# Kernel optimization log

Hardware: AMD Instinct MI355X
Metric: run time of the kernel (lower is better)

## Reference

```python
import jax, jax.numpy as jnp
import numpy as np

D_MODEL = 1024
D_STATE = 16  # hardcoded in original: A = randn(d_model, 16)


def setup_inputs() -> dict:
    key = jax.random.key(0)
    ks = jax.random.split(key, 9)
    D = D_MODEL
    s = 1.0 / np.sqrt(D)
    x = jax.random.normal(ks[0], (4, 8192, D), dtype=jnp.float32)
    in_w = jax.random.uniform(ks[1], (2 * D, D), minval=-s, maxval=s, dtype=jnp.float32)
    in_b = jax.random.uniform(ks[2], (2 * D,), minval=-s, maxval=s, dtype=jnp.float32)
    out_w = jax.random.uniform(ks[3], (D, D), minval=-s, maxval=s, dtype=jnp.float32)
    out_b = jax.random.uniform(ks[4], (D,), minval=-s, maxval=s, dtype=jnp.float32)
    dt_w = jax.random.uniform(ks[5], (D, D), minval=-s, maxval=s, dtype=jnp.float32)
    dt_b = jax.random.uniform(ks[6], (D,), minval=-s, maxval=s, dtype=jnp.float32)
    A = jax.random.normal(ks[7], (D, D_STATE), dtype=jnp.float32)
    Dp = jax.random.normal(ks[8], (D,), dtype=jnp.float32)
    return {"x": x, "in_w": in_w, "in_b": in_b, "out_w": out_w, "out_b": out_b,
            "dt_w": dt_w, "dt_b": dt_b, "A": A, "Dp": Dp}


def reference(x, in_w, in_b, out_w, out_b, dt_w, dt_b, A, Dp):
    # x: [B, L, D]. in_proj -> [B, L, 2D], split into x_val / res.
    x_and_res = jnp.einsum('bld,ed->ble', x, in_w) + in_b
    x_val, res = jnp.split(x_and_res, 2, axis=-1)
    # Original computes dt = softplus(dt_proj(xt)) per timestep but never uses it
    # (dead compute, A/Dp/h also unused); output depends only on silu gating.
    # y_t = xt * sigmoid(xt) == silu(x_val), fully parallel over L (no recurrence).
    y = x_val * jax.nn.sigmoid(x_val)
    gated = y * jax.nn.silu(res)
    return jnp.einsum('bld,ed->ble', gated, out_w) + out_b
```

## Files before the change

kernel.cpp:

```cpp
#include <hip/hip_runtime.h>
#include <cstdint>


typedef __bf16 bf16x8 __attribute__((ext_vector_type(8)));
typedef float f32x4 __attribute__((ext_vector_type(4)));

#define KD 1024
#define NT 32
#define BUF_ELEMS 16384

__device__ __forceinline__ void gload_lds16(const void* g, void* lds_u) {
  __builtin_amdgcn_global_load_lds(
      (__attribute__((address_space(1))) void*)(uintptr_t)g,
      (__attribute__((address_space(3))) void*)(uint32_t)(uintptr_t)lds_u,
      16, 0, 0);
}

__device__ __forceinline__ float silu_f(float v) {
  return v / (1.0f + __expf(-v));
}

#define WAITB(N) do { \
  asm volatile("s_waitcnt vmcnt(" #N ")" ::: "memory"); \
  asm volatile("s_barrier" ::: "memory"); } while (0)

__global__ void cast_f32_to_bf16_x8(const float* __restrict__ in,
                                    __bf16* __restrict__ out, int n8) {
  int i = blockIdx.x * blockDim.x + threadIdx.x;
  if (i >= n8) return;
  const float4* p = (const float4*)in;
  float4 v0 = p[2 * i];
  float4 v1 = p[2 * i + 1];
  bf16x8 o;
  o[0] = (__bf16)v0.x; o[1] = (__bf16)v0.y; o[2] = (__bf16)v0.z; o[3] = (__bf16)v0.w;
  o[4] = (__bf16)v1.x; o[5] = (__bf16)v1.y; o[6] = (__bf16)v1.z; o[7] = (__bf16)v1.w;
  ((bf16x8*)out)[i] = o;
}

__global__ void cast_w1_interleave(const float* __restrict__ in,
                                   __bf16* __restrict__ out) {
  int i = blockIdx.x * blockDim.x + threadIdx.x;
  int orow = i >> 7;
  int chunk = i & 127;
  int srow = (orow >> 1) + ((orow & 1) << 10);
  const float4* p = (const float4*)(in + ((size_t)srow << 10) + (chunk << 3));
  float4 v0 = p[0], v1 = p[1];
  bf16x8 o;
  o[0] = (__bf16)v0.x; o[1] = (__bf16)v0.y; o[2] = (__bf16)v0.z; o[3] = (__bf16)v0.w;
  o[4] = (__bf16)v1.x; o[5] = (__bf16)v1.y; o[6] = (__bf16)v1.z; o[7] = (__bf16)v1.w;
  *(bf16x8*)(out + ((size_t)orow << 10) + (chunk << 3)) = o;
}

template <int BUF>
__device__ __forceinline__ void stage_tile(const __bf16*& pa, const __bf16*& pb,
                                           __bf16* smw) {
  __bf16* d = smw + BUF * BUF_ELEMS;
  gload_lds16(pa, d);
  gload_lds16(pa + 128 * KD, d + 4096);
  gload_lds16(pb, d + 8192);
  gload_lds16(pb + 128 * KD, d + 12288);
  pa += 32;
  pb += 32;
}

template <int BUF>
__device__ __forceinline__ void compute_tile(const __bf16* sm, int aoff, int boff,
                                             f32x4 (&acc)[8][4]) {
  const __bf16* base = sm + BUF * BUF_ELEMS;
  bf16x8 af[8], bf[4];
#pragma unroll
  for (int i = 0; i < 8; ++i)
    af[i] = *(const bf16x8*)(base + aoff + i * 512);
#pragma unroll
  for (int j = 0; j < 4; ++j)
    bf[j] = *(const bf16x8*)(base + boff + j * 512);
  __builtin_amdgcn_s_setprio(1);
#pragma unroll
  for (int i = 0; i < 8; ++i)
#pragma unroll
    for (int j = 0; j < 4; ++j)
      acc[i][j] = __builtin_amdgcn_mfma_f32_16x16x32_bf16(af[i], bf[j], acc[i][j], 0, 0, 0);
  __builtin_amdgcn_s_setprio(0);
}

__device__ __forceinline__ void gemm_core(const __bf16* __restrict__ A,
                                          const __bf16* __restrict__ B,
                                          __bf16* sm, long m0, long n0,
                                          f32x4 (&acc)[8][4]) {
  const int t = threadIdx.x;
  const int w = t >> 6;
  const int lane = t & 63;
  const int lr = lane & 15;
  const int lk = lane >> 4;
  const int wr = w >> 2;
  const int wc = w & 3;

  const int l = lane;
  const int stg_row = w * 16 + (l >> 2);
  const int stg_col = ((l & 3) ^ ((l >> 3) & 3)) << 3;
  const __bf16* pa = A + (m0 + stg_row) * KD + stg_col;
  const __bf16* pb = B + (n0 + stg_row) * KD + stg_col;
  __bf16* smw = sm + w * 512;

  const int swz8 = (lk ^ ((lr >> 1) & 3)) << 3;
  const int aoff = (wr * 128 + lr) * 32 + swz8;
  const int boff = 8192 + (wc * 64 + lr) * 32 + swz8;

#pragma unroll
  for (int i = 0; i < 8; ++i)
#pragma unroll
    for (int j = 0; j < 4; ++j)
      acc[i][j] = (f32x4){0.f, 0.f, 0.f, 0.f};

  stage_tile<0>(pa, pb, smw);
  stage_tile<1>(pa, pb, smw);

  for (int it = 0; it < 10; ++it) {
    WAITB(4); stage_tile<2>(pa, pb, smw); compute_tile<0>(sm, aoff, boff, acc);
    WAITB(4); stage_tile<0>(pa, pb, smw); compute_tile<1>(sm, aoff, boff, acc);
    WAITB(4); stage_tile<1>(pa, pb, smw); compute_tile<2>(sm, aoff, boff, acc);
  }
  WAITB(4); compute_tile<0>(sm, aoff, boff, acc);
  WAITB(0); compute_tile<1>(sm, aoff, boff, acc);
}

__global__ __launch_bounds__(512, 2)
void gemm1_silu(const __bf16* __restrict__ X, const __bf16* __restrict__ W1i,
                const float* __restrict__ in_b, __bf16* __restrict__ G) {
  __shared__ __bf16 sm[3 * BUF_ELEMS];
  const int bid = blockIdx.x;
  const int swz = (bid & 7) * 128 + (bid >> 3);
  const int m_idx = swz >> 3;
  const int n_idx = swz & 7;
  const long m0 = (long)m_idx * 256;
  const long n0 = (long)n_idx * 256;

  f32x4 acc[8][4];
  gemm_core(X, W1i, sm, m0, n0, acc);

  const int lane = threadIdx.x & 63;
  const int w = threadIdx.x >> 6;
  const int wr = w >> 2, wc = w & 3;

  float bj[4];
#pragma unroll
  for (int j = 0; j < 4; ++j) {
    int nn = (int)n0 + wc * 64 + j * 16 + (lane & 15);
    bj[j] = (nn & 1) ? in_b[1024 + (nn >> 1)] : in_b[nn >> 1];
  }
#pragma unroll
  for (int i = 0; i < 8; ++i)
#pragma unroll
    for (int j = 0; j < 4; ++j)
#pragma unroll
      for (int q = 0; q < 4; ++q) {
        int r = wr * 128 + i * 16 + (lane >> 4) * 4 + q;
        float v = acc[i][j][q] + bj[j];
        float s = silu_f(v);
        float p = __shfl_xor(s, 1);
        float g = s * p;
        if (!(lane & 1)) {
          int nn = (int)n0 + wc * 64 + j * 16 + (lane & 15);
          G[(m0 + r) * 1024 + (nn >> 1)] = (__bf16)g;
        }
      }
}

__global__ __launch_bounds__(512, 2)
void gemm2_bias(const __bf16* __restrict__ G, const __bf16* __restrict__ W2,
                const float* __restrict__ out_b, float* __restrict__ OUT) {
  __shared__ __bf16 sm[3 * BUF_ELEMS];
  const int bid = blockIdx.x;
  const int swz = (bid & 7) * 64 + (bid >> 3);
  const int m_idx = swz >> 2;
  const int n_idx = swz & 3;
  const long m0 = (long)m_idx * 256;
  const long n0 = (long)n_idx * 256;

  f32x4 acc[8][4];
  gemm_core(G, W2, sm, m0, n0, acc);

  const int lane = threadIdx.x & 63;
  const int w = threadIdx.x >> 6;
  const int wr = w >> 2, wc = w & 3;

  float ob[4];
#pragma unroll
  for (int j = 0; j < 4; ++j)
    ob[j] = out_b[(int)n0 + wc * 64 + j * 16 + (lane & 15)];
#pragma unroll
  for (int i = 0; i < 8; ++i)
#pragma unroll
    for (int j = 0; j < 4; ++j)
#pragma unroll
      for (int q = 0; q < 4; ++q) {
        int r = wr * 128 + i * 16 + (lane >> 4) * 4 + q;
        int c = wc * 64 + j * 16 + (lane & 15);
        OUT[(m0 + r) * 1024 + n0 + c] = acc[i][j][q] + ob[j];
      }
}

extern "C" void kernel_launch(void* const* d_in, const int* in_sizes, int n_in,
                              void* d_out, int out_size, void* d_ws, size_t ws_size,
                              hipStream_t stream) {
  const float* x = (const float*)d_in[0];
  const float* in_w = (const float*)d_in[1];
  const float* in_b = (const float*)d_in[2];
  const float* out_w = (const float*)d_in[3];
  const float* out_b = (const float*)d_in[4];

  char* ws = (char*)d_ws;
  __bf16* xb = (__bf16*)(ws);
  __bf16* w1b = (__bf16*)(ws + (size_t)67108864);
  __bf16* w2b = (__bf16*)(ws + (size_t)71303168);
  __bf16* gb = (__bf16*)(ws + (size_t)73400320);

  cast_f32_to_bf16_x8<<<dim3(16384), 256, 0, stream>>>(x, xb, 33554432 / 8);
  cast_w1_interleave<<<dim3(1024), 256, 0, stream>>>(in_w, w1b);
  cast_f32_to_bf16_x8<<<dim3(512), 256, 0, stream>>>(out_w, w2b, 1048576 / 8);

  gemm1_silu<<<dim3(1024), 512, 0, stream>>>(xb, w1b, in_b, gb);
  gemm2_bias<<<dim3(512), 512, 0, stream>>>(gb, w2b, out_b, (float*)d_out);
}
```

Baseline: 291.7 us.

## Restructure GEMM mainloop to BK=64 double-buffer with phased MFMA/LDS interleave

Replaces the triple-buffered BK=32 pipeline with a double-buffered BK=64 scheme. Each K-tile is split into four barrier-delimited phases that interleave LDS fragment reads, global-to-LDS staging of the next tile, and MFMA bursts at raised priority. A new XOR swizzle fits the 64-wide rows. The aim is fewer barriers per K step and better overlap of loads with MFMA. In exchange it uses 128KB of LDS per block, which may drop the two-blocks-per-CU occupancy the launch bounds ask for, and it adds more barriers inside each tile.

After: 288.0 us. No clear change (-1.3%).

```diff
diff --git a/kernel.cpp b/kernel.cpp
--- a/kernel.cpp
+++ b/kernel.cpp
@@ -6,8 +6,6 @@
 typedef float f32x4 __attribute__((ext_vector_type(4)));
 
 #define KD 1024
-#define NT 32
-#define BUF_ELEMS 16384
 
 __device__ __forceinline__ void gload_lds16(const void* g, void* lds_u) {
   __builtin_amdgcn_global_load_lds(
@@ -19,10 +17,6 @@
 __device__ __forceinline__ float silu_f(float v) {
   return v / (1.0f + __expf(-v));
 }
-
-#define WAITB(N) do { \
-  asm volatile("s_waitcnt vmcnt(" #N ")" ::: "memory"); \
-  asm volatile("s_barrier" ::: "memory"); } while (0)
 
 __global__ void cast_f32_to_bf16_x8(const float* __restrict__ in,
                                     __bf16* __restrict__ out, int n8) {
@@ -51,36 +45,82 @@
   *(bf16x8*)(out + ((size_t)orow << 10) + (chunk << 3)) = o;
 }
 
-template <int BUF>
-__device__ __forceinline__ void stage_tile(const __bf16*& pa, const __bf16*& pb,
-                                           __bf16* smw) {
-  __bf16* d = smw + BUF * BUF_ELEMS;
-  gload_lds16(pa, d);
-  gload_lds16(pa + 128 * KD, d + 4096);
-  gload_lds16(pb, d + 8192);
-  gload_lds16(pb + 128 * KD, d + 12288);
-  pa += 32;
-  pb += 32;
-}
-
-template <int BUF>
-__device__ __forceinline__ void compute_tile(const __bf16* sm, int aoff, int boff,
-                                             f32x4 (&acc)[8][4]) {
-  const __bf16* base = sm + BUF * BUF_ELEMS;
-  bf16x8 af[8], bf[4];
-#pragma unroll
-  for (int i = 0; i < 8; ++i)
-    af[i] = *(const bf16x8*)(base + aoff + i * 512);
-#pragma unroll
-  for (int j = 0; j < 4; ++j)
-    bf[j] = *(const bf16x8*)(base + boff + j * 512);
-  __builtin_amdgcn_s_setprio(1);
-#pragma unroll
-  for (int i = 0; i < 8; ++i)
-#pragma unroll
-    for (int j = 0; j < 4; ++j)
-      acc[i][j] = __builtin_amdgcn_mfma_f32_16x16x32_bf16(af[i], bf[j], acc[i][j], 0, 0, 0);
+__device__ __forceinline__ void stage4(const __bf16* psrc, __bf16* smdst) {
+  gload_lds16(psrc,          smdst);
+  gload_lds16(psrc + 65536,  smdst + 4096);
+  gload_lds16(psrc + 131072, smdst + 8192);
+  gload_lds16(psrc + 196608, smdst + 12288);
+}
+
+#define MFMA16(I0)                                                              \
+  do {                                                                          \
+    _Pragma("unroll") for (int a2 = 0; a2 < 2; ++a2) {                          \
+      _Pragma("unroll") for (int jn = 0; jn < 4; ++jn) {                        \
+        acc[(I0) + a2][jn] = __builtin_amdgcn_mfma_f32_16x16x32_bf16(           \
+            af[a2][0], bf[jn][0], acc[(I0) + a2][jn], 0, 0, 0);                 \
+        acc[(I0) + a2][jn] = __builtin_amdgcn_mfma_f32_16x16x32_bf16(           \
+            af[a2][1], bf[jn][1], acc[(I0) + a2][jn], 0, 0, 0);                 \
+      }                                                                         \
+    }                                                                           \
+  } while (0)
+
+#define RD_A(ai, i)                                                             \
+  do {                                                                          \
+    af[ai][0] = *(const bf16x8*)(Bp + aBase + (i) * 1024 + o0);                 \
+    af[ai][1] = *(const bf16x8*)(Bp + aBase + (i) * 1024 + o1);                 \
+  } while (0)
+
+#define PH_ENTER()                                                              \
+  do {                                                                          \
+    __builtin_amdgcn_s_barrier();                                               \
+    asm volatile("s_waitcnt lgkmcnt(0)" ::: "memory");                          \
+    __builtin_amdgcn_sched_barrier(0);                                          \
+    __builtin_amdgcn_s_setprio(1);                                              \
+  } while (0)
+
+#define PH_EXIT()                                                               \
+  do {                                                                          \
+    __builtin_amdgcn_s_setprio(0);                                              \
+    __builtin_amdgcn_s_barrier();                                               \
+  } while (0)
+
+template <int BUFE>
+__device__ __forceinline__ void compute_half(
+    const __bf16* sm, int aBase, int bBase, int o0, int o1, f32x4 (&acc)[8][4],
+    const __bf16* pa_st, const __bf16* pb_st, __bf16* smA_st, __bf16* smB_st,
+    bool do_stage) {
+  const __bf16* Bp = sm + BUFE;
+  bf16x8 bf[4][2], af[2][2];
+#pragma unroll
+  for (int jn = 0; jn < 4; ++jn) {
+    bf[jn][0] = *(const bf16x8*)(Bp + bBase + jn * 1024 + o0);
+    bf[jn][1] = *(const bf16x8*)(Bp + bBase + jn * 1024 + o1);
+  }
+  RD_A(0, 0);
+  RD_A(1, 1);
+  asm volatile("s_waitcnt lgkmcnt(8)" ::: "memory");
+  if (do_stage) stage4(pa_st, smA_st);
+  PH_ENTER();
+  MFMA16(0);
+  PH_EXIT();
+  RD_A(0, 2);
+  RD_A(1, 3);
+  if (do_stage) stage4(pb_st, smB_st);
+  PH_ENTER();
+  MFMA16(2);
+  PH_EXIT();
+  RD_A(0, 4);
+  RD_A(1, 5);
+  PH_ENTER();
+  MFMA16(4);
+  PH_EXIT();
+  RD_A(0, 6);
+  RD_A(1, 7);
+  PH_ENTER();
+  MFMA16(6);
   __builtin_amdgcn_s_setprio(0);
+  asm volatile("s_waitcnt vmcnt(0)" ::: "memory");
+  __builtin_amdgcn_s_barrier();
 }
 
 __device__ __forceinline__ void gemm_core(const __bf16* __restrict__ A,
@@ -95,16 +135,21 @@
   const int wr = w >> 2;
   const int wc = w & 3;
 
-  const int l = lane;
-  const int stg_row = w * 16 + (l >> 2);
-  const int stg_col = ((l & 3) ^ ((l >> 3) & 3)) << 3;
-  const __bf16* pa = A + (m0 + stg_row) * KD + stg_col;
-  const __bf16* pb = B + (n0 + stg_row) * KD + stg_col;
-  __bf16* smw = sm + w * 512;
-
-  const int swz8 = (lk ^ ((lr >> 1) & 3)) << 3;
-  const int aoff = (wr * 128 + lr) * 32 + swz8;
-  const int boff = 8192 + (wc * 64 + lr) * 32 + swz8;
+  const int sw = lr & 7;
+  const int o0 = (lk ^ sw) << 3;
+  const int o1 = o0 ^ 32;
+  const int aBase = (wr * 128 + lr) * 64;
+  const int bBase = 16384 + (wc * 64 + lr) * 64;
+
+  const int grow = lane >> 3;
+  const int gchk = ((lane & 7) ^ grow) << 3;
+  const __bf16* pa = A + (m0 + w * 8 + grow) * KD + gchk;
+  const __bf16* pb = B + (n0 + w * 8 + grow) * KD + gchk;
+
+  __bf16* smA0 = sm + w * 512;
+  __bf16* smB0 = sm + 16384 + w * 512;
+  __bf16* smA1 = sm + 32768 + w * 512;
+  __bf16* smB1 = sm + 32768 + 16384 + w * 512;
 
 #pragma unroll
   for (int i = 0; i < 8; ++i)
@@ -112,28 +157,28 @@
     for (int j = 0; j < 4; ++j)
       acc[i][j] = (f32x4){0.f, 0.f, 0.f, 0.f};
 
-  stage_tile<0>(pa, pb, smw);
-  stage_tile<1>(pa, pb, smw);
-
-  for (int it = 0; it < 10; ++it) {
-    WAITB(4); stage_tile<2>(pa, pb, smw); compute_tile<0>(sm, aoff, boff, acc);
-    WAITB(4); stage_tile<0>(pa, pb, smw); compute_tile<1>(sm, aoff, boff, acc);
-    WAITB(4); stage_tile<1>(pa, pb, smw); compute_tile<2>(sm, aoff, boff, acc);
+  stage4(pa, smA0);
+  stage4(pb, smB0);
+  asm volatile("s_waitcnt vmcnt(0)" ::: "memory");
+  __builtin_amdgcn_s_barrier();
+
+  for (int it = 0; it < 8; ++it) {
+    compute_half<0>(sm, aBase, bBase, o0, o1, acc,
+                    pa + it * 128 + 64, pb + it * 128 + 64, smA1, smB1, true);
+    compute_half<32768>(sm, aBase, bBase, o0, o1, acc,
+                        pa + (it + 1) * 128, pb + (it + 1) * 128, smA0, smB0,
+                        it < 7);
   }
-  WAITB(4); compute_tile<0>(sm, aoff, boff, acc);
-  WAITB(0); compute_tile<1>(sm, aoff, boff, acc);
 }
 
 __global__ __launch_bounds__(512, 2)
 void gemm1_silu(const __bf16* __restrict__ X, const __bf16* __restrict__ W1i,
                 const float* __restrict__ in_b, __bf16* __restrict__ G) {
-  __shared__ __bf16 sm[3 * BUF_ELEMS];
+  __shared__ __bf16 sm[65536];
   const int bid = blockIdx.x;
   const int swz = (bid & 7) * 128 + (bid >> 3);
-  const int m_idx = swz >> 3;
-  const int n_idx = swz & 7;
-  const long m0 = (long)m_idx * 256;
-  const long n0 = (long)n_idx * 256;
+  const long m0 = (long)(swz >> 3) * 256;
+  const long n0 = (long)(swz & 7) * 256;
 
   f32x4 acc[8][4];
   gemm_core(X, W1i, sm, m0, n0, acc);
@@ -169,13 +214,11 @@
 __global__ __launch_bounds__(512, 2)
 void gemm2_bias(const __bf16* __restrict__ G, const __bf16* __restrict__ W2,
                 const float* __restrict__ out_b, float* __restrict__ OUT) {
-  __shared__ __bf16 sm[3 * BUF_ELEMS];
+  __shared__ __bf16 sm[65536];
   const int bid = blockIdx.x;
   const int swz = (bid & 7) * 64 + (bid >> 3);
-  const int m_idx = swz >> 2;
-  const int n_idx = swz & 3;
-  const long m0 = (long)m_idx * 256;
-  const long n0 = (long)n_idx * 256;
+  const long m0 = (long)(swz >> 2) * 256;
+  const long n0 = (long)(swz & 3) * 256;
 
   f32x4 acc[8][4];
   gemm_core(G, W2, sm, m0, n0, acc);
```

## Switch GEMMs to 32x32x16 MFMA and block-interleave W1 for shuffle-free gating

Applied to the files above, without the earlier changes.

Both GEMM cores now use 32x32x16 bf16 MFMA instructions with 16-wide accumulators in place of 16x16x32, with the LDS read offsets and swizzle adjusted to match. W1 is reordered in 32-row blocks, alternating x_val and res, so each lane holds matching x and res values in its two accumulator columns. The gating epilogue therefore computes silu(x)*silu(res) directly with one reciprocal and no cross-lane shuffle, and every lane stores. The larger MFMA halves the number of instructions and LDS fragment reads per tile, but changes register pressure and the store pattern.

After: 271.4 us. 7.0% less time.

```diff
diff --git a/kernel.cpp b/kernel.cpp
--- a/kernel.cpp
+++ b/kernel.cpp
@@ -3,10 +3,9 @@
 
 
 typedef __bf16 bf16x8 __attribute__((ext_vector_type(8)));
-typedef float f32x4 __attribute__((ext_vector_type(4)));
+typedef float f32x16 __attribute__((ext_vector_type(16)));
 
 #define KD 1024
-#define NT 32
 #define BUF_ELEMS 16384
 
 __device__ __forceinline__ void gload_lds16(const void* g, void* lds_u) {
@@ -14,10 +13,6 @@
       (__attribute__((address_space(1))) void*)(uintptr_t)g,
       (__attribute__((address_space(3))) void*)(uint32_t)(uintptr_t)lds_u,
       16, 0, 0);
-}
-
-__device__ __forceinline__ float silu_f(float v) {
-  return v / (1.0f + __expf(-v));
 }
 
 #define WAITB(N) do { \
@@ -37,12 +32,13 @@
   ((bf16x8*)out)[i] = o;
 }
 
-__global__ void cast_w1_interleave(const float* __restrict__ in,
-                                   __bf16* __restrict__ out) {
+__global__ void cast_w1_blk32(const float* __restrict__ in,
+                              __bf16* __restrict__ out) {
   int i = blockIdx.x * blockDim.x + threadIdx.x;
   int orow = i >> 7;
   int chunk = i & 127;
-  int srow = (orow >> 1) + ((orow & 1) << 10);
+  int b = orow >> 5, t = orow & 31;
+  int srow = (b & 1) * 1024 + (b >> 1) * 32 + t;
   const float4* p = (const float4*)(in + ((size_t)srow << 10) + (chunk << 3));
   float4 v0 = p[0], v1 = p[1];
   bf16x8 o;
@@ -64,34 +60,45 @@
 }
 
 template <int BUF>
-__device__ __forceinline__ void compute_tile(const __bf16* sm, int aoff, int boff,
-                                             f32x4 (&acc)[8][4]) {
+__device__ __forceinline__ void compute_tile(const __bf16* sm,
+                                             int aoff0, int aoff1,
+                                             int boff0, int boff1,
+                                             f32x16 (&acc)[4][2]) {
   const __bf16* base = sm + BUF * BUF_ELEMS;
-  bf16x8 af[8], bf[4];
-#pragma unroll
-  for (int i = 0; i < 8; ++i)
-    af[i] = *(const bf16x8*)(base + aoff + i * 512);
-#pragma unroll
-  for (int j = 0; j < 4; ++j)
-    bf[j] = *(const bf16x8*)(base + boff + j * 512);
+  bf16x8 a0[4], a1[4], b0[2], b1[2];
+#pragma unroll
+  for (int j = 0; j < 2; ++j) {
+    b0[j] = *(const bf16x8*)(base + boff0 + j * 1024);
+    b1[j] = *(const bf16x8*)(base + boff1 + j * 1024);
+  }
+#pragma unroll
+  for (int i = 0; i < 4; ++i) {
+    a0[i] = *(const bf16x8*)(base + aoff0 + i * 1024);
+    a1[i] = *(const bf16x8*)(base + aoff1 + i * 1024);
+  }
   __builtin_amdgcn_s_setprio(1);
 #pragma unroll
-  for (int i = 0; i < 8; ++i)
-#pragma unroll
-    for (int j = 0; j < 4; ++j)
-      acc[i][j] = __builtin_amdgcn_mfma_f32_16x16x32_bf16(af[i], bf[j], acc[i][j], 0, 0, 0);
+  for (int i = 0; i < 4; ++i)
+#pragma unroll
+    for (int j = 0; j < 2; ++j)
+      acc[i][j] = __builtin_amdgcn_mfma_f32_32x32x16_bf16(a0[i], b0[j], acc[i][j], 0, 0, 0);
+#pragma unroll
+  for (int i = 0; i < 4; ++i)
+#pragma unroll
+    for (int j = 0; j < 2; ++j)
+      acc[i][j] = __builtin_amdgcn_mfma_f32_32x32x16_bf16(a1[i], b1[j], acc[i][j], 0, 0, 0);
   __builtin_amdgcn_s_setprio(0);
 }
 
 __device__ __forceinline__ void gemm_core(const __bf16* __restrict__ A,
                                           const __bf16* __restrict__ B,
                                           __bf16* sm, long m0, long n0,
-                                          f32x4 (&acc)[8][4]) {
+                                          f32x16 (&acc)[4][2]) {
   const int t = threadIdx.x;
   const int w = t >> 6;
   const int lane = t & 63;
-  const int lr = lane & 15;
-  const int lk = lane >> 4;
+  const int c31 = lane & 31;
+  const int hi = lane >> 5;
   const int wr = w >> 2;
   const int wc = w & 3;
 
@@ -102,26 +109,34 @@
   const __bf16* pb = B + (n0 + stg_row) * KD + stg_col;
   __bf16* smw = sm + w * 512;
 
-  const int swz8 = (lk ^ ((lr >> 1) & 3)) << 3;
-  const int aoff = (wr * 128 + lr) * 32 + swz8;
-  const int boff = 8192 + (wc * 64 + lr) * 32 + swz8;
-
-#pragma unroll
-  for (int i = 0; i < 8; ++i)
-#pragma unroll
-    for (int j = 0; j < 4; ++j)
-      acc[i][j] = (f32x4){0.f, 0.f, 0.f, 0.f};
+  const int key = (c31 >> 1) & 3;
+  const int ch0 = (hi ^ key) << 3;
+  const int ch1 = ((2 + hi) ^ key) << 3;
+  const int aoff0 = (wr * 128 + c31) * 32 + ch0;
+  const int aoff1 = (wr * 128 + c31) * 32 + ch1;
+  const int boff0 = 8192 + (wc * 64 + c31) * 32 + ch0;
+  const int boff1 = 8192 + (wc * 64 + c31) * 32 + ch1;
+
+#pragma unroll
+  for (int i = 0; i < 4; ++i)
+#pragma unroll
+    for (int j = 0; j < 2; ++j)
+      acc[i][j] = (f32x16){0.f, 0.f, 0.f, 0.f, 0.f, 0.f, 0.f, 0.f,
+                           0.f, 0.f, 0.f, 0.f, 0.f, 0.f, 0.f, 0.f};
 
   stage_tile<0>(pa, pb, smw);
   stage_tile<1>(pa, pb, smw);
 
   for (int it = 0; it < 10; ++it) {
-    WAITB(4); stage_tile<2>(pa, pb, smw); compute_tile<0>(sm, aoff, boff, acc);
-    WAITB(4); stage_tile<0>(pa, pb, smw); compute_tile<1>(sm, aoff, boff, acc);
-    WAITB(4); stage_tile<1>(pa, pb, smw); compute_tile<2>(sm, aoff, boff, acc);
+    WAITB(4); stage_tile<2>(pa, pb, smw);
+    compute_tile<0>(sm, aoff0, aoff1, boff0, boff1, acc);
+    WAITB(4); stage_tile<0>(pa, pb, smw);
+    compute_tile<1>(sm, aoff0, aoff1, boff0, boff1, acc);
+    WAITB(4); stage_tile<1>(pa, pb, smw);
+    compute_tile<2>(sm, aoff0, aoff1, boff0, boff1, acc);
   }
-  WAITB(4); compute_tile<0>(sm, aoff, boff, acc);
-  WAITB(0); compute_tile<1>(sm, aoff, boff, acc);
+  WAITB(4); compute_tile<0>(sm, aoff0, aoff1, boff0, boff1, acc);
+  WAITB(0); compute_tile<1>(sm, aoff0, aoff1, boff0, boff1, acc);
 }
 
 __global__ __launch_bounds__(512, 2)
@@ -130,40 +145,34 @@
   __shared__ __bf16 sm[3 * BUF_ELEMS];
   const int bid = blockIdx.x;
   const int swz = (bid & 7) * 128 + (bid >> 3);
-  const int m_idx = swz >> 3;
-  const int n_idx = swz & 7;
-  const long m0 = (long)m_idx * 256;
-  const long n0 = (long)n_idx * 256;
-
-  f32x4 acc[8][4];
+  const long m0 = (long)(swz >> 3) * 256;
+  const long n0 = (long)(swz & 7) * 256;
+
+  f32x16 acc[4][2];
   gemm_core(X, W1i, sm, m0, n0, acc);
 
   const int lane = threadIdx.x & 63;
   const int w = threadIdx.x >> 6;
   const int wr = w >> 2, wc = w & 3;
-
-  float bj[4];
-#pragma unroll
-  for (int j = 0; j < 4; ++j) {
-    int nn = (int)n0 + wc * 64 + j * 16 + (lane & 15);
-    bj[j] = (nn & 1) ? in_b[1024 + (nn >> 1)] : in_b[nn >> 1];
-  }
-#pragma unroll
-  for (int i = 0; i < 8; ++i)
-#pragma unroll
-    for (int j = 0; j < 4; ++j)
-#pragma unroll
-      for (int q = 0; q < 4; ++q) {
-        int r = wr * 128 + i * 16 + (lane >> 4) * 4 + q;
-        float v = acc[i][j][q] + bj[j];
-        float s = silu_f(v);
-        float p = __shfl_xor(s, 1);
-        float g = s * p;
-        if (!(lane & 1)) {
-          int nn = (int)n0 + wc * 64 + j * 16 + (lane & 15);
-          G[(m0 + r) * 1024 + (nn >> 1)] = (__bf16)g;
-        }
-      }
+  const int c31 = lane & 31;
+  const int hi = lane >> 5;
+
+  const int gc = ((int)n0 >> 1) + wc * 32 + c31;
+  const float bx = in_b[gc];
+  const float br = in_b[1024 + gc];
+
+#pragma unroll
+  for (int i = 0; i < 4; ++i)
+#pragma unroll
+    for (int reg = 0; reg < 16; ++reg) {
+      const int row = wr * 128 + i * 32 + (reg & 3) + 8 * (reg >> 2) + 4 * hi;
+      float xv = acc[i][0][reg] + bx;
+      float rs = acc[i][1][reg] + br;
+      float e1 = __expf(-xv);
+      float e2 = __expf(-rs);
+      float g = xv * rs * __builtin_amdgcn_rcpf((1.0f + e1) * (1.0f + e2));
+      G[(m0 + row) * 1024 + gc] = (__bf16)g;
+    }
 }
 
 __global__ __launch_bounds__(512, 2)
@@ -172,31 +181,31 @@
   __shared__ __bf16 sm[3 * BUF_ELEMS];
   const int bid = blockIdx.x;
   const int swz = (bid & 7) * 64 + (bid >> 3);
-  const int m_idx = swz >> 2;
-  const int n_idx = swz & 3;
-  const long m0 = (long)m_idx * 256;
-  const long n0 = (long)n_idx * 256;
-
-  f32x4 acc[8][4];
+  const long m0 = (long)(swz >> 2) * 256;
+  const long n0 = (long)(swz & 3) * 256;
+
+  f32x16 acc[4][2];
   gemm_core(G, W2, sm, m0, n0, acc);
 
   const int lane = threadIdx.x & 63;
   const int w = threadIdx.x >> 6;
   const int wr = w >> 2, wc = w & 3;
-
-  float ob[4];
-#pragma unroll
-  for (int j = 0; j < 4; ++j)
-    ob[j] = out_b[(int)n0 + wc * 64 + j * 16 + (lane & 15)];
-#pragma unroll
-  for (int i = 0; i < 8; ++i)
-#pragma unroll
-    for (int j = 0; j < 4; ++j)
-#pragma unroll
-      for (int q = 0; q < 4; ++q) {
-        int r = wr * 128 + i * 16 + (lane >> 4) * 4 + q;
-        int c = wc * 64 + j * 16 + (lane & 15);
-        OUT[(m0 + r) * 1024 + n0 + c] = acc[i][j][q] + ob[j];
+  const int c31 = lane & 31;
+  const int hi = lane >> 5;
+
+  float ob[2];
+#pragma unroll
+  for (int j = 0; j < 2; ++j)
+    ob[j] = out_b[(int)n0 + wc * 64 + j * 32 + c31];
+#pragma unroll
+  for (int i = 0; i < 4; ++i)
+#pragma unroll
+    for (int j = 0; j < 2; ++j)
+#pragma unroll
+      for (int reg = 0; reg < 16; ++reg) {
+        const int row = wr * 128 + i * 32 + (reg & 3) + 8 * (reg >> 2) + 4 * hi;
+        const int col = (int)n0 + wc * 64 + j * 32 + c31;
+        OUT[(m0 + row) * 1024 + col] = acc[i][j][reg] + ob[j];
       }
 }
 
@@ -216,7 +225,7 @@
   __bf16* gb = (__bf16*)(ws + (size_t)73400320);
 
   cast_f32_to_bf16_x8<<<dim3(16384), 256, 0, stream>>>(x, xb, 33554432 / 8);
-  cast_w1_interleave<<<dim3(1024), 256, 0, stream>>>(in_w, w1b);
+  cast_w1_blk32<<<dim3(1024), 256, 0, stream>>>(in_w, w1b);
   cast_f32_to_bf16_x8<<<dim3(512), 256, 0, stream>>>(out_w, w2b, 1048576 / 8);
 
   gemm1_silu<<<dim3(1024), 512, 0, stream>>>(xb, w1b, in_b, gb);
```
